# Kernel tuning notes

Measured on AMD Instinct MI355X. Metric: run time of the kernel, lower is better.

## Reference

```python
import jax, jax.numpy as jnp
import numpy as np

NUM_GRAPHS = 64
HID = 6
NUM_CLASSES = 10
NUM_FEATS = 128


def setup_inputs() -> dict:
    key = jax.random.key(0)
    ks = jax.random.split(key, 20)
    N, E = 100000, 3200000
    x = jax.random.normal(ks[0], (N, NUM_FEATS), dtype=jnp.float32)
    edge_index = jax.random.randint(ks[1], (2, E), 0, N, dtype=jnp.int64)
    batch = jnp.sort(jax.random.randint(ks[2], (N,), 0, NUM_GRAPHS, dtype=jnp.int64))
    def glorot(k, fan_in, fan_out):
        lim = np.sqrt(6.0 / (fan_in + fan_out))
        return jax.random.uniform(k, (fan_in, fan_out), jnp.float32, -lim, lim)
    inp = {"x": x, "edge_index": edge_index, "batch": batch}
    dims = [(NUM_FEATS, HID)] + [(HID, HID)] * 5 + [(HID, NUM_CLASSES)]
    names = ["1", "2", "3", "4", "5", "6", "f"]
    for i, (nm, (fi, fo)) in enumerate(zip(names, dims)):
        inp["W" + nm] = glorot(ks[3 + i], fi, fo)
        inp["b" + nm] = jnp.zeros((fo,), jnp.float32)
    return inp


def _gcn_forward(x, edge_index, batch, Ws, bs):
    N = x.shape[0]
    loop = jnp.arange(N, dtype=edge_index.dtype)
    src = jnp.concatenate([edge_index[0], loop])  # self-loops appended
    dst = jnp.concatenate([edge_index[1], loop])
    deg = jax.ops.segment_sum(jnp.ones_like(dst, dtype=x.dtype), dst, num_segments=N)
    dinv = jnp.where(deg > 0, jax.lax.rsqrt(deg), 0.0)
    norm = dinv[src] * dinv[dst]  # [E+N]

    def conv(h, W, b):
        h = h @ W  # [N, out]
        agg = jax.ops.segment_sum(h[src] * norm[:, None], dst, num_segments=N)
        return agg + b

    h = x
    for W, b in zip(Ws, bs):
        h = jax.nn.relu(conv(h, W, b))

    # global mean pool over graphs
    sums = jax.ops.segment_sum(h, batch, num_segments=NUM_GRAPHS)
    cnts = jax.ops.segment_sum(jnp.ones((N,), h.dtype), batch, num_segments=NUM_GRAPHS)
    pooled = sums / jnp.maximum(cnts, 1.0)[:, None]
    return jax.nn.log_softmax(pooled, axis=1)


def reference(x, edge_index, batch, W1, b1, W2, b2, W3, b3, W4, b4, W5, b5, W6, b6, Wf, bf):
    Ws = [W1, W2, W3, W4, W5, W6, Wf]
    bs = [b1, b2, b3, b4, b5, b6, bf]
    return _gcn_forward(x, edge_index, batch, Ws, bs)
```

## Files before the change

### kernel.cpp

```cpp
#include <hip/hip_runtime.h>
#include <hip/hip_bf16.h>
#include <hip/hip_fp16.h>
#include <math.h>

#define NF     128
#define HID    6
#define NC     10
#define NG     64
#define SLOTS  64
#define OVFCAP 8192

#define BKT_SH    7
#define BKT_NODES 128
#define NBK_MAX   1024
#define EPB       4096
#define BCAP      5120
#define BOVFCAP   4096

__device__ __forceinline__ void addh2(__half2& a0, __half2& a1, __half2& a2, uint4 q) {
    const __half2* h = (const __half2*)&q;
    a0 = __hadd2(a0, h[0]);
    a1 = __hadd2(a1, h[1]);
    a2 = __hadd2(a2, h[2]);
}

__device__ __forceinline__ __half2 shfl_xor_h2(__half2 v, int m) {
    union { __half2 h; unsigned int u; } a;
    a.h = v;
    a.u = __shfl_xor(a.u, m);
    return a.h;
}

__device__ __forceinline__ uint4 packh(const float* v) {
    uint4 q;
    __half2* h = (__half2*)&q;
    h[0] = __floats2half2_rn(v[0], v[1]);
    h[1] = __floats2half2_rn(v[2], v[3]);
    h[2] = __floats2half2_rn(v[4], v[5]);
    h[3] = __floats2half2_rn(0.f, 0.f);
    return q;
}

__global__ __launch_bounds__(256) void bucket_scatter_kernel(
        const int* __restrict__ src, const int* __restrict__ dst, int E, int nbk,
        int* __restrict__ bucket_cursor, unsigned int* __restrict__ bucket_arr,
        int* __restrict__ bovf_meta, int2* __restrict__ bovf) {
    __shared__ int cntL[NBK_MAX];
    __shared__ int gb[NBK_MAX];
    int tid = threadIdx.x;
    for (int k = tid; k < NBK_MAX; k += 256) cntL[k] = 0;
    __syncthreads();
    int e0 = blockIdx.x * EPB;
    int cnt_e = E - e0; if (cnt_e > EPB) cnt_e = EPB;
    int sreg[16], dreg[16], rank[16];
    if (cnt_e == EPB && (E & 3) == 0) {
        const int4* s4p = (const int4*)(src + e0);
        const int4* d4p = (const int4*)(dst + e0);
#pragma unroll
        for (int k = 0; k < 4; ++k) {
            int4 sv = s4p[k * 256 + tid];
            int4 dv = d4p[k * 256 + tid];
            sreg[4*k+0] = sv.x; sreg[4*k+1] = sv.y; sreg[4*k+2] = sv.z; sreg[4*k+3] = sv.w;
            dreg[4*k+0] = dv.x; dreg[4*k+1] = dv.y; dreg[4*k+2] = dv.z; dreg[4*k+3] = dv.w;
        }
#pragma unroll
        for (int k = 0; k < 16; ++k) rank[k] = atomicAdd(&cntL[dreg[k] >> BKT_SH], 1);
    } else {
#pragma unroll
        for (int k = 0; k < 16; ++k) {
            int e = e0 + k * 256 + tid;
            if (e < E) {
                dreg[k] = dst[e]; sreg[k] = src[e];
                rank[k] = atomicAdd(&cntL[dreg[k] >> BKT_SH], 1);
            } else dreg[k] = -1;
        }
    }
    __syncthreads();
    for (int bb = tid; bb < nbk; bb += 256) {
        int c = cntL[bb];
        if (c > 0) gb[bb] = atomicAdd(&bucket_cursor[bb], c);
    }
    __syncthreads();
#pragma unroll
    for (int k = 0; k < 16; ++k) {
        int d = dreg[k];
        if (d < 0) continue;
        int b = d >> BKT_SH;
        unsigned int p = (unsigned int)(d & (BKT_NODES - 1)) | ((unsigned int)sreg[k] << BKT_SH);
        int grel = gb[b] + rank[k];
        if (grel < BCAP) {
            bucket_arr[(size_t)b * BCAP + grel] = p;
        } else {
            int p2 = atomicAdd(bovf_meta, 1);
            if (p2 < BOVFCAP) bovf[p2] = make_int2(d, sreg[k]);
        }
    }
}

__global__ __launch_bounds__(256) void ell_build_kernel(
        const unsigned int* __restrict__ bucket_arr, const int* __restrict__ bucket_cursor,
        const int* __restrict__ bovf_meta, const int2* __restrict__ bovf,
        int* __restrict__ ell, int* __restrict__ cnt, float* __restrict__ dinv,
        int* __restrict__ ovf_meta, int* __restrict__ ovf_dst, int* __restrict__ ovf_src,
        int N) {
    __shared__ int ell_s[BKT_NODES * SLOTS];
    __shared__ int cur[BKT_NODES];
    int b = blockIdx.x;
    int tid = threadIdx.x;
    if (tid < BKT_NODES) cur[tid] = 0;
    for (int k = tid; k < BKT_NODES * SLOTS; k += 256) ell_s[k] = N;
    __syncthreads();
    int bc = bucket_cursor[b];
    if (bc > BCAP) bc = BCAP;
    const unsigned int* ba = bucket_arr + (size_t)b * BCAP;
    for (int j = tid; j < bc; j += 256) {
        unsigned int p = ba[j];
        int r = (int)(p & (BKT_NODES - 1));
        int s = (int)(p >> BKT_SH);
        int slot = atomicAdd(&cur[r], 1);
        if (slot < SLOTS) {
            ell_s[r * SLOTS + slot] = s;
        } else {
            int d = (b << BKT_SH) + r;
            int q = atomicAdd(ovf_meta, 1);
            if (q < OVFCAP) { ovf_dst[q] = d; ovf_src[q] = s; }
        }
    }
    int m = *bovf_meta;
    if (m > BOVFCAP) m = BOVFCAP;
    for (int t = tid; t < m; t += 256) {
        int2 e = bovf[t];
        if ((e.x >> BKT_SH) == b) {
            int r = e.x & (BKT_NODES - 1);
            int slot = atomicAdd(&cur[r], 1);
            if (slot < SLOTS) {
                ell_s[r * SLOTS + slot] = e.y;
            } else {
                int q = atomicAdd(ovf_meta, 1);
                if (q < OVFCAP) { ovf_dst[q] = e.x; ovf_src[q] = e.y; }
            }
        }
    }
    __syncthreads();
    int nid0 = b << BKT_SH;
    int rows = N - nid0; if (rows > BKT_NODES) rows = BKT_NODES;
    if (rows <= 0) return;
    int4* eg = (int4*)(ell + (size_t)nid0 * SLOTS);
    const int4* es = (const int4*)ell_s;
    for (int k = tid; k < rows * (SLOTS / 4); k += 256) {
        int r = k >> 4;
        int q = k & 15;
        int c = cur[r]; if (c > SLOTS) c = SLOTS;
        if (q * 4 < c) eg[k] = es[k];
    }
    for (int r = tid; r < rows; r += 256) {
        int deg = cur[r];
        cnt[nid0 + r] = deg;
        dinv[nid0 + r] = rsqrtf((float)deg + 1.0f);
    }
}

__global__ __launch_bounds__(256) void layer1_kernel(const float* __restrict__ x,
                                                     const float* __restrict__ W,
                                                     const float* __restrict__ dinv,
                                                     uint4* __restrict__ g16, int N) {
    __shared__ float sW[8 * 100];
    for (int idx = threadIdx.x; idx < NF * HID; idx += 256) {
        int s = idx / 96, r = idx % 96;
        int o = r / 16, j = r % 16;
        sW[s * 100 + o * 16 + j] = W[(s * 16 + j) * HID + o];
    }
    __syncthreads();
    int t = blockIdx.x * 256 + threadIdx.x;
    int i = t >> 3;
    int sub = t & 7;
    if (t == 0) g16[N] = make_uint4(0u, 0u, 0u, 0u);
    if (i >= N) return;
    const float4* xr = (const float4*)(x + (size_t)i * NF + sub * 16);
    float4 xv0 = xr[0], xv1 = xr[1], xv2 = xr[2], xv3 = xr[3];
    const float4* wr = (const float4*)(sW + sub * 100);
    float p[HID];
#pragma unroll
    for (int o = 0; o < HID; ++o) {
        float4 w0 = wr[o * 4 + 0], w1 = wr[o * 4 + 1], w2 = wr[o * 4 + 2], w3 = wr[o * 4 + 3];
        p[o] = xv0.x * w0.x + xv0.y * w0.y + xv0.z * w0.z + xv0.w * w0.w
             + xv1.x * w1.x + xv1.y * w1.y + xv1.z * w1.z + xv1.w * w1.w
             + xv2.x * w2.x + xv2.y * w2.y + xv2.z * w2.z + xv2.w * w2.w
             + xv3.x * w3.x + xv3.y * w3.y + xv3.z * w3.z + xv3.w * w3.w;
    }
#pragma unroll
    for (int m = 1; m < 8; m <<= 1) {
#pragma unroll
        for (int o = 0; o < HID; ++o) p[o] += __shfl_xor(p[o], m);
    }
    if (sub == 0) {
        float dv = dinv[i];
        float v[HID];
#pragma unroll
        for (int o = 0; o < HID; ++o) v[o] = dv * p[o];
        g16[i] = packh(v);
    }
}

__device__ __forceinline__ void gather8h(int ne, const int* __restrict__ er,
                                         const uint4* __restrict__ g16, int sub,
                                         __half2& a0, __half2& a1, __half2& a2) {
#pragma unroll
    for (int r = 0; r < SLOTS / 32; ++r) {
        int base = r * 32 + sub * 4;
        if (base < ne) {
            int4 q = *(const int4*)(er + base);
            uint4 v0 = g16[q.x];
            uint4 v1 = g16[q.y];
            uint4 v2 = g16[q.z];
            uint4 v3 = g16[q.w];
            addh2(a0, a1, a2, v0);
            addh2(a0, a1, a2, v1);
            addh2(a0, a1, a2, v2);
            addh2(a0, a1, a2, v3);
        }
    }
}

template<int PREP>
__global__ __launch_bounds__(256) void gcn_layer8_kernel(
        const int* __restrict__ cnt, const int* __restrict__ ell,
        const int* __restrict__ ovf_meta, const int* __restrict__ ovf_dst,
        const int* __restrict__ ovf_src, const float* __restrict__ dinv,
        const uint4* __restrict__ gin, uint4* __restrict__ gout,
        const float* __restrict__ W, const float* __restrict__ b, int N) {
    int t = blockIdx.x * 256 + threadIdx.x;
    int i = t >> 3;
    int sub = t & 7;
    if (t == 0) gout[N] = make_uint4(0u, 0u, 0u, 0u);
    if (i >= N) return;
    int n = cnt[i];
    int ne = n < SLOTS ? n : SLOTS;
    const int* er = ell + (size_t)i * SLOTS;
    __half2 a0 = __float2half2_rn(0.f), a1 = a0, a2 = a0;
    gather8h(ne, er, gin, sub, a0, a1, a2);
    if (sub == 0) addh2(a0, a1, a2, gin[i]);
    if (n > SLOTS && sub == 2) {
        int m = ovf_meta[0];
        m = m < OVFCAP ? m : OVFCAP;
        for (int tt = 0; tt < m; ++tt) {
            if (ovf_dst[tt] == i) addh2(a0, a1, a2, gin[ovf_src[tt]]);
        }
    }
#pragma unroll
    for (int m = 1; m < 8; m <<= 1) {
        a0 = __hadd2(a0, shfl_xor_h2(a0, m));
        a1 = __hadd2(a1, shfl_xor_h2(a1, m));
        a2 = __hadd2(a2, shfl_xor_h2(a2, m));
    }
    if (sub != 0) return;
    float2 f0 = __half22float2(a0), f1 = __half22float2(a1), f2 = __half22float2(a2);
    float acc[HID] = { f0.x, f0.y, f1.x, f1.y, f2.x, f2.y };
    float dv = dinv[i];
    float h[HID];
#pragma unroll
    for (int f = 0; f < HID; ++f) {
        float u = dv * acc[f] + b[f];
        h[f] = u > 0.0f ? u : 0.0f;
    }
    float o[HID];
    if (PREP) {
#pragma unroll
        for (int f = 0; f < HID; ++f) o[f] = dv * h[f];
    } else {
#pragma unroll
        for (int fo = 0; fo < HID; ++fo) {
            float s = 0.0f;
#pragma unroll
            for (int fi = 0; fi < HID; ++fi) s += h[fi] * W[fi * HID + fo];
            o[fo] = dv * s;
        }
    }
    gout[i] = packh(o);
}

__global__ __launch_bounds__(256) void pool_kernel(
        const int* __restrict__ cnt, const int* __restrict__ ell,
        const int* __restrict__ ovf_meta, const int* __restrict__ ovf_dst,
        const int* __restrict__ ovf_src, const float* __restrict__ dinv,
        const uint4* __restrict__ gin, const int* __restrict__ batch,
        const float* __restrict__ Wf, const float* __restrict__ bf,
        float* __restrict__ pooled, float* __restrict__ gcnt, int N) {
    __shared__ float sp[NG * NC];
    __shared__ float sc[NG];
    __shared__ int srange[2];
    for (int k = threadIdx.x; k < NG * NC; k += 256) sp[k] = 0.0f;
    if (threadIdx.x < NG) sc[threadIdx.x] = 0.0f;
    int start = blockIdx.x * 32;
    int endi = min(start + 32, N) - 1;
    if (threadIdx.x == 0) {
        srange[0] = batch[start];
        srange[1] = batch[endi];
    }
    __syncthreads();
    int t = blockIdx.x * 256 + threadIdx.x;
    int i = t >> 3;
    int sub = t & 7;
    if (i < N) {
        int n = cnt[i];
        int ne = n < SLOTS ? n : SLOTS;
        const int* er = ell + (size_t)i * SLOTS;
        __half2 a0 = __float2half2_rn(0.f), a1 = a0, a2 = a0;
        gather8h(ne, er, gin, sub, a0, a1, a2);
        if (sub == 0) addh2(a0, a1, a2, gin[i]);
        if (n > SLOTS && sub == 2) {
            int m = ovf_meta[0];
            m = m < OVFCAP ? m : OVFCAP;
            for (int tt = 0; tt < m; ++tt) {
                if (ovf_dst[tt] == i) addh2(a0, a1, a2, gin[ovf_src[tt]]);
            }
        }
#pragma unroll
        for (int m = 1; m < 8; m <<= 1) {
            a0 = __hadd2(a0, shfl_xor_h2(a0, m));
            a1 = __hadd2(a1, shfl_xor_h2(a1, m));
            a2 = __hadd2(a2, shfl_xor_h2(a2, m));
        }
        if (sub == 0) {
            float2 f0 = __half22float2(a0), f1 = __half22float2(a1), f2 = __half22float2(a2);
            float acc[HID] = { f0.x, f0.y, f1.x, f1.y, f2.x, f2.y };
            float dv = dinv[i];
            float u[HID];
#pragma unroll
            for (int f = 0; f < HID; ++f) u[f] = dv * acc[f];
            int bg = batch[i];
#pragma unroll
            for (int c = 0; c < NC; ++c) {
                float v = bf[c];
#pragma unroll
                for (int f = 0; f < HID; ++f) v += u[f] * Wf[f * NC + c];
                v = v > 0.0f ? v : 0.0f;
                atomicAdd(&sp[bg * NC + c], v);
            }
            atomicAdd(&sc[bg], 1.0f);
        }
    }
    __syncthreads();
    int bmin = srange[0], bmax = srange[1];
    int rows = bmax - bmin + 1;
    for (int k = threadIdx.x; k < rows * NC; k += 256) {
        int r = bmin + k / NC, c = k % NC;
        float v = sp[r * NC + c];
        if (v != 0.0f) atomicAdd(&pooled[r * NC + c], v);
    }
    for (int k = threadIdx.x; k < rows; k += 256) {
        float v = sc[bmin + k];
        if (v != 0.0f) atomicAdd(&gcnt[bmin + k], v);
    }
}

__global__ void logsm_kernel(const float* __restrict__ pooled, const float* __restrict__ gcnt,
                             float* __restrict__ out) {
    int gidx = threadIdx.x;
    if (gidx >= NG) return;
    float c = gcnt[gidx];
    c = c > 1.0f ? c : 1.0f;
    float v[NC];
    float m = -1e30f;
#pragma unroll
    for (int k = 0; k < NC; ++k) {
        v[k] = pooled[gidx * NC + k] / c;
        m = v[k] > m ? v[k] : m;
    }
    float s = 0.0f;
#pragma unroll
    for (int k = 0; k < NC; ++k) s += expf(v[k] - m);
    float ls = logf(s);
#pragma unroll
    for (int k = 0; k < NC; ++k) out[gidx * NC + k] = v[k] - m - ls;
}

extern "C" void kernel_launch(void* const* d_in, const int* in_sizes, int n_in,
                              void* d_out, int out_size, void* d_ws, size_t ws_size,
                              hipStream_t stream) {
    const float* x     = (const float*)d_in[0];
    const int*   ei    = (const int*)d_in[1];
    const int*   batch = (const int*)d_in[2];
    const float* W[7];
    const float* b[7];
    for (int l = 0; l < 7; ++l) {
        W[l] = (const float*)d_in[3 + 2 * l];
        b[l] = (const float*)d_in[4 + 2 * l];
    }
    const int N = in_sizes[2];
    const int E = in_sizes[1] / 2;
    const int nbk = (N + BKT_NODES - 1) >> BKT_SH;
    const int* src = ei;
    const int* dst = ei + E;
    float* out = (float*)d_out;

    char* wp = (char*)d_ws;
    int* bucket_cursor = (int*)wp;  wp += (size_t)NBK_MAX * 4;
    int* ovf_meta  = (int*)wp;      wp += 16;
    int* bovf_meta = (int*)wp;      wp += 16;
    int* ovf_dst   = (int*)wp;      wp += OVFCAP * 4;
    int* ovf_src   = (int*)wp;      wp += OVFCAP * 4;
    int2* bovf     = (int2*)wp;     wp += (size_t)BOVFCAP * 8;
    int* cnt       = (int*)wp;      wp += (((size_t)N * 4 + 15) & ~15ull);
    float* dinv    = (float*)wp;    wp += (((size_t)N * 4 + 15) & ~15ull);
    uint4* g_a     = (uint4*)wp;    wp += (size_t)(N + 1) * 16;
    uint4* g_b     = (uint4*)wp;    wp += (size_t)(N + 1) * 16;
    float* pooled  = (float*)wp;    wp += NG * NC * 4;
    float* gcnt    = (float*)wp;    wp += (((size_t)NG * 4 + 15) & ~15ull);
    int* ell       = (int*)wp;      wp += (size_t)N * SLOTS * 4;
    unsigned int* bucket_arr = (unsigned int*)wp;  wp += (size_t)nbk * BCAP * 4;

    hipMemsetAsync(bucket_cursor, 0, (size_t)NBK_MAX * 4 + 32, stream);
    hipMemsetAsync(pooled, 0, (NG * NC + NG) * sizeof(float), stream);

    const int BT = 256;
    int bn8 = ((size_t)N * 8 + BT - 1) / BT;
    int bp1 = (E + EPB - 1) / EPB;

    bucket_scatter_kernel<<<bp1, BT, 0, stream>>>(src, dst, E, nbk, bucket_cursor,
                                                  bucket_arr, bovf_meta, bovf);
    ell_build_kernel<<<nbk, BT, 0, stream>>>(bucket_arr, bucket_cursor, bovf_meta, bovf,
                                             ell, cnt, dinv, ovf_meta, ovf_dst, ovf_src, N);

    layer1_kernel<<<bn8, BT, 0, stream>>>(x, W[0], dinv, g_a, N);

    gcn_layer8_kernel<0><<<bn8, BT, 0, stream>>>(cnt, ell, ovf_meta, ovf_dst, ovf_src, dinv, g_a, g_b, W[1], b[0], N);
    gcn_layer8_kernel<0><<<bn8, BT, 0, stream>>>(cnt, ell, ovf_meta, ovf_dst, ovf_src, dinv, g_b, g_a, W[2], b[1], N);
    gcn_layer8_kernel<0><<<bn8, BT, 0, stream>>>(cnt, ell, ovf_meta, ovf_dst, ovf_src, dinv, g_a, g_b, W[3], b[2], N);
    gcn_layer8_kernel<0><<<bn8, BT, 0, stream>>>(cnt, ell, ovf_meta, ovf_dst, ovf_src, dinv, g_b, g_a, W[4], b[3], N);
    gcn_layer8_kernel<0><<<bn8, BT, 0, stream>>>(cnt, ell, ovf_meta, ovf_dst, ovf_src, dinv, g_a, g_b, W[5], b[4], N);
    gcn_layer8_kernel<1><<<bn8, BT, 0, stream>>>(cnt, ell, ovf_meta, ovf_dst, ovf_src, dinv, g_b, g_a, nullptr, b[5], N);
    pool_kernel<<<bn8, BT, 0, stream>>>(cnt, ell, ovf_meta, ovf_dst, ovf_src, dinv, g_a, batch, W[6], b[6], pooled, gcnt, N);
    logsm_kernel<<<1, 64, 0, stream>>>(pooled, gcnt, out);
}
```

Baseline: 353.8 us.

## Build ELL adjacency with direct global atomics instead of two-pass bucketing

Replaces the two-kernel bucket scatter plus shared-memory ELL build with a single kernel that does a global atomicAdd on each destination's counter and writes the source straight into its ELL slot. dinv is now computed inside layer1 from the counts. Unfilled ELL slots are no longer padded, so the gather masks out-of-range lanes to the zero row N. This drops one kernel launch and the bucket array traffic, at the cost of 3.2M scattered global atomics and uncoalesced 4-byte ELL writes.

```diff
diff --git a/kernel.cpp b/kernel.cpp
--- a/kernel.cpp
+++ b/kernel.cpp
@@ -10,12 +10,6 @@
 #define SLOTS  64
 #define OVFCAP 8192
 
-#define BKT_SH    7
-#define BKT_NODES 128
-#define NBK_MAX   1024
-#define EPB       4096
-#define BCAP      5120
-#define BOVFCAP   4096
 
 __device__ __forceinline__ void addh2(__half2& a0, __half2& a1, __half2& a2, uint4 q) {
     const __half2* h = (const __half2*)&q;
@@ -41,128 +35,49 @@
     return q;
 }
 
-__global__ __launch_bounds__(256) void bucket_scatter_kernel(
-        const int* __restrict__ src, const int* __restrict__ dst, int E, int nbk,
-        int* __restrict__ bucket_cursor, unsigned int* __restrict__ bucket_arr,
-        int* __restrict__ bovf_meta, int2* __restrict__ bovf) {
-    __shared__ int cntL[NBK_MAX];
-    __shared__ int gb[NBK_MAX];
-    int tid = threadIdx.x;
-    for (int k = tid; k < NBK_MAX; k += 256) cntL[k] = 0;
-    __syncthreads();
-    int e0 = blockIdx.x * EPB;
-    int cnt_e = E - e0; if (cnt_e > EPB) cnt_e = EPB;
-    int sreg[16], dreg[16], rank[16];
-    if (cnt_e == EPB && (E & 3) == 0) {
-        const int4* s4p = (const int4*)(src + e0);
-        const int4* d4p = (const int4*)(dst + e0);
+__global__ __launch_bounds__(256) void edge_scatter_kernel(
+        const int* __restrict__ src, const int* __restrict__ dst, int E,
+        int* __restrict__ cnt, int* __restrict__ ell,
+        int* __restrict__ ovf_meta, int* __restrict__ ovf_dst, int* __restrict__ ovf_src) {
+    int t = blockIdx.x * 256 + threadIdx.x;
+    int stride = gridDim.x * 256;
+    int nq = E >> 2;
+    const int4* s4 = (const int4*)src;
+    const int4* d4 = (const int4*)dst;
+    for (int q = t; q < nq; q += stride) {
+        int4 sv = s4[q];
+        int4 dv = d4[q];
+        int ss[4] = { sv.x, sv.y, sv.z, sv.w };
+        int dd[4] = { dv.x, dv.y, dv.z, dv.w };
 #pragma unroll
         for (int k = 0; k < 4; ++k) {
-            int4 sv = s4p[k * 256 + tid];
-            int4 dv = d4p[k * 256 + tid];
-            sreg[4*k+0] = sv.x; sreg[4*k+1] = sv.y; sreg[4*k+2] = sv.z; sreg[4*k+3] = sv.w;
-            dreg[4*k+0] = dv.x; dreg[4*k+1] = dv.y; dreg[4*k+2] = dv.z; dreg[4*k+3] = dv.w;
-        }
-#pragma unroll
-        for (int k = 0; k < 16; ++k) rank[k] = atomicAdd(&cntL[dreg[k] >> BKT_SH], 1);
-    } else {
-#pragma unroll
-        for (int k = 0; k < 16; ++k) {
-            int e = e0 + k * 256 + tid;
-            if (e < E) {
-                dreg[k] = dst[e]; sreg[k] = src[e];
-                rank[k] = atomicAdd(&cntL[dreg[k] >> BKT_SH], 1);
-            } else dreg[k] = -1;
-        }
-    }
-    __syncthreads();
-    for (int bb = tid; bb < nbk; bb += 256) {
-        int c = cntL[bb];
-        if (c > 0) gb[bb] = atomicAdd(&bucket_cursor[bb], c);
-    }
-    __syncthreads();
-#pragma unroll
-    for (int k = 0; k < 16; ++k) {
-        int d = dreg[k];
-        if (d < 0) continue;
-        int b = d >> BKT_SH;
-        unsigned int p = (unsigned int)(d & (BKT_NODES - 1)) | ((unsigned int)sreg[k] << BKT_SH);
-        int grel = gb[b] + rank[k];
-        if (grel < BCAP) {
-            bucket_arr[(size_t)b * BCAP + grel] = p;
+            int d = dd[k];
+            int slot = atomicAdd(&cnt[d], 1);
+            if (slot < SLOTS) {
+                ell[(size_t)d * SLOTS + slot] = ss[k];
+            } else {
+                int p = atomicAdd(ovf_meta, 1);
+                if (p < OVFCAP) { ovf_dst[p] = d; ovf_src[p] = ss[k]; }
+            }
+        }
+    }
+    for (int e = (nq << 2) + t; e < E; e += stride) {
+        int d = dst[e];
+        int s = src[e];
+        int slot = atomicAdd(&cnt[d], 1);
+        if (slot < SLOTS) {
+            ell[(size_t)d * SLOTS + slot] = s;
         } else {
-            int p2 = atomicAdd(bovf_meta, 1);
-            if (p2 < BOVFCAP) bovf[p2] = make_int2(d, sreg[k]);
-        }
-    }
-}
-
-__global__ __launch_bounds__(256) void ell_build_kernel(
-        const unsigned int* __restrict__ bucket_arr, const int* __restrict__ bucket_cursor,
-        const int* __restrict__ bovf_meta, const int2* __restrict__ bovf,
-        int* __restrict__ ell, int* __restrict__ cnt, float* __restrict__ dinv,
-        int* __restrict__ ovf_meta, int* __restrict__ ovf_dst, int* __restrict__ ovf_src,
-        int N) {
-    __shared__ int ell_s[BKT_NODES * SLOTS];
-    __shared__ int cur[BKT_NODES];
-    int b = blockIdx.x;
-    int tid = threadIdx.x;
-    if (tid < BKT_NODES) cur[tid] = 0;
-    for (int k = tid; k < BKT_NODES * SLOTS; k += 256) ell_s[k] = N;
-    __syncthreads();
-    int bc = bucket_cursor[b];
-    if (bc > BCAP) bc = BCAP;
-    const unsigned int* ba = bucket_arr + (size_t)b * BCAP;
-    for (int j = tid; j < bc; j += 256) {
-        unsigned int p = ba[j];
-        int r = (int)(p & (BKT_NODES - 1));
-        int s = (int)(p >> BKT_SH);
-        int slot = atomicAdd(&cur[r], 1);
-        if (slot < SLOTS) {
-            ell_s[r * SLOTS + slot] = s;
-        } else {
-            int d = (b << BKT_SH) + r;
-            int q = atomicAdd(ovf_meta, 1);
-            if (q < OVFCAP) { ovf_dst[q] = d; ovf_src[q] = s; }
-        }
-    }
-    int m = *bovf_meta;
-    if (m > BOVFCAP) m = BOVFCAP;
-    for (int t = tid; t < m; t += 256) {
-        int2 e = bovf[t];
-        if ((e.x >> BKT_SH) == b) {
-            int r = e.x & (BKT_NODES - 1);
-            int slot = atomicAdd(&cur[r], 1);
-            if (slot < SLOTS) {
-                ell_s[r * SLOTS + slot] = e.y;
-            } else {
-                int q = atomicAdd(ovf_meta, 1);
-                if (q < OVFCAP) { ovf_dst[q] = e.x; ovf_src[q] = e.y; }
-            }
-        }
-    }
-    __syncthreads();
-    int nid0 = b << BKT_SH;
-    int rows = N - nid0; if (rows > BKT_NODES) rows = BKT_NODES;
-    if (rows <= 0) return;
-    int4* eg = (int4*)(ell + (size_t)nid0 * SLOTS);
-    const int4* es = (const int4*)ell_s;
-    for (int k = tid; k < rows * (SLOTS / 4); k += 256) {
-        int r = k >> 4;
-        int q = k & 15;
-        int c = cur[r]; if (c > SLOTS) c = SLOTS;
-        if (q * 4 < c) eg[k] = es[k];
-    }
-    for (int r = tid; r < rows; r += 256) {
-        int deg = cur[r];
-        cnt[nid0 + r] = deg;
-        dinv[nid0 + r] = rsqrtf((float)deg + 1.0f);
+            int p = atomicAdd(ovf_meta, 1);
+            if (p < OVFCAP) { ovf_dst[p] = d; ovf_src[p] = s; }
+        }
     }
 }
 
 __global__ __launch_bounds__(256) void layer1_kernel(const float* __restrict__ x,
                                                      const float* __restrict__ W,
-                                                     const float* __restrict__ dinv,
+                                                     const int* __restrict__ cnt,
+                                                     float* __restrict__ dinv,
                                                      uint4* __restrict__ g16, int N) {
     __shared__ float sW[8 * 100];
     for (int idx = threadIdx.x; idx < NF * HID; idx += 256) {
@@ -194,7 +109,8 @@
         for (int o = 0; o < HID; ++o) p[o] += __shfl_xor(p[o], m);
     }
     if (sub == 0) {
-        float dv = dinv[i];
+        float dv = rsqrtf((float)cnt[i] + 1.0f);
+        dinv[i] = dv;
         float v[HID];
 #pragma unroll
         for (int o = 0; o < HID; ++o) v[o] = dv * p[o];
@@ -203,17 +119,20 @@
 }
 
 __device__ __forceinline__ void gather8h(int ne, const int* __restrict__ er,
-                                         const uint4* __restrict__ g16, int sub,
+                                         const uint4* __restrict__ g16, int sub, int N,
                                          __half2& a0, __half2& a1, __half2& a2) {
 #pragma unroll
     for (int r = 0; r < SLOTS / 32; ++r) {
         int base = r * 32 + sub * 4;
         if (base < ne) {
             int4 q = *(const int4*)(er + base);
+            int i1 = (base + 1 < ne) ? q.y : N;
+            int i2 = (base + 2 < ne) ? q.z : N;
+            int i3 = (base + 3 < ne) ? q.w : N;
             uint4 v0 = g16[q.x];
-            uint4 v1 = g16[q.y];
-            uint4 v2 = g16[q.z];
-            uint4 v3 = g16[q.w];
+            uint4 v1 = g16[i1];
+            uint4 v2 = g16[i2];
+            uint4 v3 = g16[i3];
             addh2(a0, a1, a2, v0);
             addh2(a0, a1, a2, v1);
             addh2(a0, a1, a2, v2);
@@ -238,7 +157,7 @@
     int ne = n < SLOTS ? n : SLOTS;
     const int* er = ell + (size_t)i * SLOTS;
     __half2 a0 = __float2half2_rn(0.f), a1 = a0, a2 = a0;
-    gather8h(ne, er, gin, sub, a0, a1, a2);
+    gather8h(ne, er, gin, sub, N, a0, a1, a2);
     if (sub == 0) addh2(a0, a1, a2, gin[i]);
     if (n > SLOTS && sub == 2) {
         int m = ovf_meta[0];
@@ -306,7 +225,7 @@
         int ne = n < SLOTS ? n : SLOTS;
         const int* er = ell + (size_t)i * SLOTS;
         __half2 a0 = __float2half2_rn(0.f), a1 = a0, a2 = a0;
-        gather8h(ne, er, gin, sub, a0, a1, a2);
+        gather8h(ne, er, gin, sub, N, a0, a1, a2);
         if (sub == 0) addh2(a0, a1, a2, gin[i]);
         if (n > SLOTS && sub == 2) {
             int m = ovf_meta[0];
@@ -389,40 +308,34 @@
     }
     const int N = in_sizes[2];
     const int E = in_sizes[1] / 2;
-    const int nbk = (N + BKT_NODES - 1) >> BKT_SH;
     const int* src = ei;
     const int* dst = ei + E;
     float* out = (float*)d_out;
 
     char* wp = (char*)d_ws;
-    int* bucket_cursor = (int*)wp;  wp += (size_t)NBK_MAX * 4;
+    int* cnt       = (int*)wp;      wp += (((size_t)N * 4 + 15) & ~15ull);
     int* ovf_meta  = (int*)wp;      wp += 16;
-    int* bovf_meta = (int*)wp;      wp += 16;
     int* ovf_dst   = (int*)wp;      wp += OVFCAP * 4;
     int* ovf_src   = (int*)wp;      wp += OVFCAP * 4;
-    int2* bovf     = (int2*)wp;     wp += (size_t)BOVFCAP * 8;
-    int* cnt       = (int*)wp;      wp += (((size_t)N * 4 + 15) & ~15ull);
     float* dinv    = (float*)wp;    wp += (((size_t)N * 4 + 15) & ~15ull);
     uint4* g_a     = (uint4*)wp;    wp += (size_t)(N + 1) * 16;
     uint4* g_b     = (uint4*)wp;    wp += (size_t)(N + 1) * 16;
     float* pooled  = (float*)wp;    wp += NG * NC * 4;
     float* gcnt    = (float*)wp;    wp += (((size_t)NG * 4 + 15) & ~15ull);
     int* ell       = (int*)wp;      wp += (size_t)N * SLOTS * 4;
-    unsigned int* bucket_arr = (unsigned int*)wp;  wp += (size_t)nbk * BCAP * 4;
-
-    hipMemsetAsync(bucket_cursor, 0, (size_t)NBK_MAX * 4 + 32, stream);
+
+    hipMemsetAsync(cnt, 0, (((size_t)N * 4 + 15) & ~15ull) + 16, stream);
     hipMemsetAsync(pooled, 0, (NG * NC + NG) * sizeof(float), stream);
 
     const int BT = 256;
     int bn8 = ((size_t)N * 8 + BT - 1) / BT;
-    int bp1 = (E + EPB - 1) / EPB;
-
-    bucket_scatter_kernel<<<bp1, BT, 0, stream>>>(src, dst, E, nbk, bucket_cursor,
-                                                  bucket_arr, bovf_meta, bovf);
-    ell_build_kernel<<<nbk, BT, 0, stream>>>(bucket_arr, bucket_cursor, bovf_meta, bovf,
-                                             ell, cnt, dinv, ovf_meta, ovf_dst, ovf_src, N);
-
-    layer1_kernel<<<bn8, BT, 0, stream>>>(x, W[0], dinv, g_a, N);
+    int bes = ((E >> 2) + BT - 1) / BT;
+    if (bes < 1) bes = 1;
+
+    edge_scatter_kernel<<<bes, BT, 0, stream>>>(src, dst, E, cnt, ell,
+                                                ovf_meta, ovf_dst, ovf_src);
+
+    layer1_kernel<<<bn8, BT, 0, stream>>>(x, W[0], cnt, dinv, g_a, N);
 
     gcn_layer8_kernel<0><<<bn8, BT, 0, stream>>>(cnt, ell, ovf_meta, ovf_dst, ovf_src, dinv, g_a, g_b, W[1], b[0], N);
     gcn_layer8_kernel<0><<<bn8, BT, 0, stream>>>(cnt, ell, ovf_meta, ovf_dst, ovf_src, dinv, g_b, g_a, W[2], b[1], N);
```

Measured after the change: 552.7 us. 1.56x slower.
